# Kernel tuning notes

Measured on AMD Instinct MI355X. Metric: run time of the kernel, lower is better.

## Reference

```python
import jax, jax.numpy as jnp
import numpy as np

B, H = 2048, 1024
P_DROP = 0.6


def setup_inputs() -> dict:
    key = jax.random.key(0)
    ks = jax.random.split(key, 17)
    stdv = 1.0 / np.sqrt(H)
    u = lambda k, shape: jax.random.uniform(k, shape, jnp.float32, -stdv, stdv)
    inp = {
        'input': jax.random.normal(ks[0], (B, H), jnp.float32),
        'hidden': jax.random.normal(ks[1], (B, H), jnp.float32),
        'pre_cell': jax.random.normal(ks[2], (B, H), jnp.float32),
        # weights are (hidden_size, input_size) and used as input @ W (requires H == input_size)
        'w_i': u(ks[3], (H, H)), 'w_f': u(ks[4], (H, H)),
        'w_o': u(ks[5], (H, H)), 'w_c': u(ks[6], (H, H)),
        'u_i': u(ks[7], (H, H)), 'u_f': u(ks[8], (H, H)),
        'u_o': u(ks[9], (H, H)), 'u_c': u(ks[10], (H, H)),
        'bias1': u(ks[11], (H,)), 'bias2': u(ks[12], (H,)),
        'bias3': u(ks[13], (H,)), 'bias4': u(ks[14], (H,)),
    }
    # F.dropout(training=True) mask, pre-scaled by 1/(1-p); shape matches h_t [B,1,H]
    keep = jax.random.bernoulli(ks[15], 1.0 - P_DROP, (B, 1, H))
    inp['drop_mask'] = keep.astype(jnp.float32) / (1.0 - P_DROP)
    return inp


def reference(input, hidden, pre_cell, w_i, w_f, w_o, w_c, u_i, u_f, u_o, u_c,
              bias1, bias2, bias3, bias4, drop_mask):
    # Fuse the 8 small GEMMs into 2 big ones: gate order (f, i, o, c)
    Wx = jnp.concatenate([w_f, w_i, w_o, w_c], axis=1)   # [H, 4H]
    Wh = jnp.concatenate([u_f, u_i, u_o, u_c], axis=1)   # [H, 4H]
    b = jnp.concatenate([bias1, bias2, bias3, bias4])    # [4H]
    gates = input @ Wx + hidden @ Wh + b                 # [B, 4H]
    f_t, i_t, o_t, g_t = jnp.split(gates, 4, axis=1)
    f_t = jax.nn.sigmoid(f_t)
    i_t = jax.nn.sigmoid(i_t)
    o_t = jax.nn.sigmoid(o_t)
    g_t = jnp.tanh(g_t)
    c_t = pre_cell * f_t + i_t * g_t                     # [B, H]
    h_t = o_t * jnp.tanh(c_t)                            # [B, H]
    h_t = h_t[:, None, :] * drop_mask                    # dropout (training=True)
    c_t = c_t[:, None, :]
    return h_t, c_t
```

## Files before the change

### kernel.cpp

```cpp
#include <hip/hip_runtime.h>
#include <hip/hip_bf16.h>
#include <cstdint>

#define B_DIM 2048
#define H_DIM 1024
#define K_DIM 2048
#define N_DIM 4096

typedef unsigned short u16;
typedef __attribute__((ext_vector_type(8))) short bf16x8;
typedef __attribute__((ext_vector_type(8))) unsigned short u16x8;
typedef __attribute__((ext_vector_type(4))) float f32x4;

__device__ __forceinline__ u16 f2bf(float f) {
    unsigned int u = __float_as_uint(f);
    u += 0x7FFFu + ((u >> 16) & 1u);
    return (u16)(u >> 16);
}

__device__ __forceinline__ float sigmoid_f(float x) {
    return 1.0f / (1.0f + __expf(-x));
}

__device__ __forceinline__ float tanh_f(float x) {
    float e = __expf(2.0f * x);
    return 1.0f - 2.0f / (e + 1.0f);
}

__device__ __forceinline__ void async16(const u16* g, u16* l) {
    __builtin_amdgcn_global_load_lds(
        (const __attribute__((address_space(1))) unsigned int*)g,
        (__attribute__((address_space(3))) unsigned int*)l,
        16, 0, 0);
}

__global__ __launch_bounds__(256) void pack_all(
    const float* __restrict__ input, const float* __restrict__ hidden,
    const float* __restrict__ w_f, const float* __restrict__ w_i,
    const float* __restrict__ w_o, const float* __restrict__ w_c,
    const float* __restrict__ u_f, const float* __restrict__ u_i,
    const float* __restrict__ u_o, const float* __restrict__ u_c,
    const float* __restrict__ b1, const float* __restrict__ b2,
    const float* __restrict__ b3, const float* __restrict__ b4,
    u16* __restrict__ A, u16* __restrict__ Bt, float* __restrict__ bias_il) {
    __shared__ float tile[32][65];
    const int blk = blockIdx.x;
    const int t = threadIdx.x;

    if (blk < 4096) {
        int idx = (blk * 256 + t) * 4;
        int m = idx >> 11;
        int k = idx & (K_DIM - 1);
        const float* src = (k < H_DIM) ? (input + (size_t)m * H_DIM + k)
                                       : (hidden + (size_t)m * H_DIM + (k - H_DIM));
        float4 v = *(const float4*)src;
        ushort4 o;
        o.x = f2bf(v.x); o.y = f2bf(v.y); o.z = f2bf(v.z); o.w = f2bf(v.w);
        *(ushort4*)(A + idx) = o;
    } else if (blk < 8192) {
        int b2i = blk - 4096;
        int z = b2i >> 9;
        int rem = b2i & 511;
        int hx = rem & 31;
        int ky = rem >> 5;
        const float* M;
        switch (z) {
            case 0: M = w_f; break;
            case 1: M = w_i; break;
            case 2: M = w_o; break;
            case 3: M = w_c; break;
            case 4: M = u_f; break;
            case 5: M = u_i; break;
            case 6: M = u_o; break;
            default: M = u_c; break;
        }
        const int g = z & 3;
        const int half = z >> 2;
        const int h0 = hx * 32;
        const int k0 = ky * 64;
#pragma unroll
        for (int it = 0; it < 2; it++) {
            int kl = (t >> 3) + it * 32;
            int hl = (t & 7) * 4;
            float4 v = *(const float4*)(M + (size_t)(k0 + kl) * H_DIM + h0 + hl);
            tile[hl + 0][kl] = v.x;
            tile[hl + 1][kl] = v.y;
            tile[hl + 2][kl] = v.z;
            tile[hl + 3][kl] = v.w;
        }
        __syncthreads();
        int hl = t >> 3;
        int ko = (t & 7) * 8;
        u16x8 o;
#pragma unroll
        for (int q = 0; q < 8; q++) o[q] = f2bf(tile[hl][ko + q]);
        size_t n = 4 * (size_t)(h0 + hl) + g;
        *(u16x8*)(Bt + n * K_DIM + half * H_DIM + k0 + ko) = o;
    } else {
        int idx = (blk - 8192) * 256 + t;
        int h = idx >> 2, g = idx & 3;
        const float* b = (g == 0) ? b1 : (g == 1) ? b2 : (g == 2) ? b3 : b4;
        bias_il[idx] = b[h];
    }
}

#define BM 128
#define BN 128
#define BK 128
#define SL (64 * 32)

__global__ __launch_bounds__(256, 2) void gemm_fused(
    const u16* __restrict__ A, const u16* __restrict__ Bt,
    const float* __restrict__ bias_il, const float* __restrict__ pre_cell,
    const float* __restrict__ mask, float* __restrict__ out) {
    __shared__ char smem[65536];
    float* et = (float*)smem;

    const int t = threadIdx.x;
    const int w = t >> 6, l = t & 63;
    const int m0 = blockIdx.y * BM;
    const int n0 = blockIdx.x * BN;
    const int wr = w >> 1;
    const int wc = w & 1;
    const int lrow = l & 15;
    const int quad = l >> 4;

    const int sr = w * 16 + (l >> 2);
    const int sc = (l & 3) * 8;
    const u16* Ag0 = A + (size_t)(m0 + sr) * K_DIM + sc;
    const u16* Ag1 = Ag0 + (size_t)64 * K_DIM;
    const u16* Bg0 = Bt + (size_t)(n0 + sr) * K_DIM + sc;
    const u16* Bg1 = Bg0 + (size_t)64 * K_DIM;
    const int soff = sr * 32 + sc;

    const int foA = (wr * 64 + lrow) * 32 + quad * 8;
    const int foB = (wc * 64 + lrow) * 32 + quad * 8;

    f32x4 acc[4][4];
#pragma unroll
    for (int j = 0; j < 4; j++) {
        float bv = bias_il[n0 + wc * 64 + j * 16 + lrow];
#pragma unroll
        for (int i = 0; i < 4; i++) acc[i][j] = (f32x4){bv, bv, bv, bv};
    }

#define COMPUTE(Asb, Bsb)                                                   \
    {                                                                       \
        bf16x8 af[4], bf[4];                                                \
        _Pragma("unroll") for (int i = 0; i < 4; i++)                       \
            af[i] = *(const bf16x8*)((Asb) + foA + i * 16 * 32);            \
        _Pragma("unroll") for (int j = 0; j < 4; j++)                       \
            bf[j] = *(const bf16x8*)((Bsb) + foB + j * 16 * 32);            \
        _Pragma("unroll") for (int i = 0; i < 4; i++)                       \
            _Pragma("unroll") for (int j = 0; j < 4; j++)                   \
                acc[i][j] = __builtin_amdgcn_mfma_f32_16x16x32_bf16(        \
                    af[i], bf[j], acc[i][j], 0, 0, 0);                      \
    }

    for (int k0 = 0; k0 < K_DIM; k0 += BK) {
        __syncthreads();
#pragma unroll
        for (int s = 0; s < 4; s++) {
            u16* Asl = (u16*)(smem + s * 8192);
            u16* Bsl = (u16*)(smem + 32768 + s * 8192);
            async16(Ag0 + k0 + s * 32, Asl + soff);
            async16(Ag1 + k0 + s * 32, Asl + soff + SL);
            async16(Bg0 + k0 + s * 32, Bsl + soff);
            async16(Bg1 + k0 + s * 32, Bsl + soff + SL);
        }
        __syncthreads();
#pragma unroll
        for (int s = 0; s < 4; s++) {
            const u16* Asl = (const u16*)(smem + s * 8192);
            const u16* Bsl = (const u16*)(smem + 32768 + s * 8192);
            COMPUTE(Asl, Bsl);
        }
    }
#undef COMPUTE

    const int row = t >> 1;
    const int half = t & 1;
    const size_t orow = (size_t)(m0 + row) * H_DIM;

    float4 pc[4], mk[4];
#pragma unroll
    for (int j = 0; j < 4; j++) {
        const int hg0 = (n0 >> 2) + half * 16 + j * 4;
        pc[j] = *(const float4*)(pre_cell + orow + hg0);
        mk[j] = *(const float4*)(mask + orow + hg0);
    }

#pragma unroll
    for (int j = 0; j < 4; j++) {
        __syncthreads();
#pragma unroll
        for (int i = 0; i < 4; i++)
#pragma unroll
            for (int r = 0; r < 4; r++)
                et[(wr * 64 + i * 16 + quad * 4 + r) * 33 + wc * 16 + lrow] =
                    acc[i][j][r];
        __syncthreads();
        const int hg0 = (n0 >> 2) + half * 16 + j * 4;
        const float* ep = et + row * 33 + half * 16;
        const float* ppc = (const float*)&pc[j];
        const float* pmk = (const float*)&mk[j];
        float4 oh, oc;
        float* poh = (float*)&oh;
        float* poc = (float*)&oc;
#pragma unroll
        for (int q = 0; q < 4; q++) {
            float fv = sigmoid_f(ep[4 * q + 0]);
            float iv = sigmoid_f(ep[4 * q + 1]);
            float ov = sigmoid_f(ep[4 * q + 2]);
            float gv = tanh_f(ep[4 * q + 3]);
            float cv = ppc[q] * fv + iv * gv;
            poc[q] = cv;
            poh[q] = ov * tanh_f(cv) * pmk[q];
        }
        *(float4*)(out + orow + hg0) = oh;
        *(float4*)(out + (size_t)B_DIM * H_DIM + orow + hg0) = oc;
    }
}

extern "C" void kernel_launch(void* const* d_in, const int* in_sizes, int n_in,
                              void* d_out, int out_size, void* d_ws, size_t ws_size,
                              hipStream_t stream) {
    const float* input    = (const float*)d_in[0];
    const float* hidden   = (const float*)d_in[1];
    const float* pre_cell = (const float*)d_in[2];
    const float* w_i = (const float*)d_in[3];
    const float* w_f = (const float*)d_in[4];
    const float* w_o = (const float*)d_in[5];
    const float* w_c = (const float*)d_in[6];
    const float* u_i = (const float*)d_in[7];
    const float* u_f = (const float*)d_in[8];
    const float* u_o = (const float*)d_in[9];
    const float* u_c = (const float*)d_in[10];
    const float* b1  = (const float*)d_in[11];
    const float* b2  = (const float*)d_in[12];
    const float* b3  = (const float*)d_in[13];
    const float* b4  = (const float*)d_in[14];
    const float* mask = (const float*)d_in[15];
    float* out = (float*)d_out;

    char* ws = (char*)d_ws;
    u16*   A       = (u16*)ws;
    u16*   Bt      = (u16*)(ws + (size_t)8 * 1024 * 1024);
    float* bias_il = (float*)(ws + (size_t)24 * 1024 * 1024);

    pack_all<<<dim3(4096 + 4096 + 16), dim3(256), 0, stream>>>(
        input, hidden, w_f, w_i, w_o, w_c, u_f, u_i, u_o, u_c,
        b1, b2, b3, b4, A, Bt, bias_il);
    gemm_fused<<<dim3(N_DIM / BN, B_DIM / BM), dim3(256), 0, stream>>>(
        A, Bt, bias_il, pre_cell, mask, out);
}
```

Baseline: 164.6 us.

## Double-buffer LDS tiles to overlap global loads with MFMA compute

```diff
diff --git a/kernel.cpp b/kernel.cpp
--- a/kernel.cpp
+++ b/kernel.cpp
@@ -32,6 +32,10 @@
         (const __attribute__((address_space(1))) unsigned int*)g,
         (__attribute__((address_space(3))) unsigned int*)l,
         16, 0, 0);
+}
+
+__device__ __forceinline__ void drain_vmem() {
+    __builtin_amdgcn_s_waitcnt(0x0F70);
 }
 
 __global__ __launch_bounds__(256) void pack_all(
@@ -106,7 +110,7 @@
 
 #define BM 128
 #define BN 128
-#define BK 128
+#define BK 64
 #define SL (64 * 32)
 
 __global__ __launch_bounds__(256, 2) void gemm_fused(
@@ -114,6 +118,14 @@
     const float* __restrict__ bias_il, const float* __restrict__ pre_cell,
     const float* __restrict__ mask, float* __restrict__ out) {
     __shared__ char smem[65536];
+    u16* A0L = (u16*)smem;
+    u16* A0H = (u16*)(smem + 8192);
+    u16* B0L = (u16*)(smem + 16384);
+    u16* B0H = (u16*)(smem + 24576);
+    u16* A1L = (u16*)(smem + 32768);
+    u16* A1H = (u16*)(smem + 40960);
+    u16* B1L = (u16*)(smem + 49152);
+    u16* B1H = (u16*)(smem + 57344);
     float* et = (float*)smem;
 
     const int t = threadIdx.x;
@@ -144,38 +156,48 @@
         for (int i = 0; i < 4; i++) acc[i][j] = (f32x4){bv, bv, bv, bv};
     }
 
-#define COMPUTE(Asb, Bsb)                                                   \
+#define STAGE(AL, AH, BL, BH, koff)              \
+    async16(Ag0 + (koff), AL + soff);            \
+    async16(Ag1 + (koff), AL + soff + SL);       \
+    async16(Ag0 + (koff) + 32, AH + soff);       \
+    async16(Ag1 + (koff) + 32, AH + soff + SL);  \
+    async16(Bg0 + (koff), BL + soff);            \
+    async16(Bg1 + (koff), BL + soff + SL);       \
+    async16(Bg0 + (koff) + 32, BH + soff);       \
+    async16(Bg1 + (koff) + 32, BH + soff + SL);
+
+#define COMPUTE(AL, AH, BL, BH)                                             \
     {                                                                       \
-        bf16x8 af[4], bf[4];                                                \
-        _Pragma("unroll") for (int i = 0; i < 4; i++)                       \
-            af[i] = *(const bf16x8*)((Asb) + foA + i * 16 * 32);            \
-        _Pragma("unroll") for (int j = 0; j < 4; j++)                       \
-            bf[j] = *(const bf16x8*)((Bsb) + foB + j * 16 * 32);            \
-        _Pragma("unroll") for (int i = 0; i < 4; i++)                       \
+        _Pragma("unroll") for (int s = 0; s < 2; s++) {                     \
+            const u16* Asb = s ? (AH) : (AL);                               \
+            const u16* Bsb = s ? (BH) : (BL);                               \
+            bf16x8 af[4], bf[4];                                            \
+            _Pragma("unroll") for (int i = 0; i < 4; i++)                   \
+                af[i] = *(const bf16x8*)(Asb + foA + i * 16 * 32);          \
             _Pragma("unroll") for (int j = 0; j < 4; j++)                   \
-                acc[i][j] = __builtin_amdgcn_mfma_f32_16x16x32_bf16(        \
-                    af[i], bf[j], acc[i][j], 0, 0, 0);                      \
-    }
-
-    for (int k0 = 0; k0 < K_DIM; k0 += BK) {
-        __syncthreads();
-#pragma unroll
-        for (int s = 0; s < 4; s++) {
-            u16* Asl = (u16*)(smem + s * 8192);
-            u16* Bsl = (u16*)(smem + 32768 + s * 8192);
-            async16(Ag0 + k0 + s * 32, Asl + soff);
-            async16(Ag1 + k0 + s * 32, Asl + soff + SL);
-            async16(Bg0 + k0 + s * 32, Bsl + soff);
-            async16(Bg1 + k0 + s * 32, Bsl + soff + SL);
-        }
-        __syncthreads();
-#pragma unroll
-        for (int s = 0; s < 4; s++) {
-            const u16* Asl = (const u16*)(smem + s * 8192);
-            const u16* Bsl = (const u16*)(smem + 32768 + s * 8192);
-            COMPUTE(Asl, Bsl);
-        }
-    }
+                bf[j] = *(const bf16x8*)(Bsb + foB + j * 16 * 32);          \
+            _Pragma("unroll") for (int i = 0; i < 4; i++)                   \
+                _Pragma("unroll") for (int j = 0; j < 4; j++)               \
+                    acc[i][j] = __builtin_amdgcn_mfma_f32_16x16x32_bf16(    \
+                        af[i], bf[j], acc[i][j], 0, 0, 0);                  \
+        }                                                                   \
+    }
+
+    STAGE(A0L, A0H, B0L, B0H, 0);
+
+    for (int k0 = 0; k0 < K_DIM; k0 += 2 * BK) {
+        drain_vmem();
+        __syncthreads();
+        STAGE(A1L, A1H, B1L, B1H, k0 + BK);
+        COMPUTE(A0L, A0H, B0L, B0H);
+        drain_vmem();
+        __syncthreads();
+        if (k0 + 2 * BK < K_DIM) {
+            STAGE(A0L, A0H, B0L, B0H, k0 + 2 * BK);
+        }
+        COMPUTE(A1L, A1H, B1L, B1H);
+    }
+#undef STAGE
 #undef COMPUTE
 
     const int row = t >> 1;
```

Result: slower. 169.4 us (+2.9%).
